# Optimization experiments

Measured on AMD Instinct MI355X. Metric: run time of the kernel, lower is better.

Reference implementation:

```python
import jax, jax.numpy as jnp
import numpy as np

DIM = 1536
HEADS = 12
HEAD_DIM = 128
SEQ = 3120
FRAME = 1560
EPS = 1e-6


def _rmsnorm(x, gamma, eps=EPS):
    var = jnp.mean(jnp.square(x), axis=-1, keepdims=True)
    return x * jax.lax.rsqrt(var + eps) * gamma


def _rope(x, cos, sin):
    # x: [B,S,H,D], cos/sin: [S, D//2]; rotate interleaved pairs (Wan-style)
    xr = x.reshape(x.shape[:-1] + (x.shape[-1] // 2, 2))
    x1, x2 = xr[..., 0], xr[..., 1]
    c = cos[None, :, None, :]
    s = sin[None, :, None, :]
    o1 = x1 * c - x2 * s
    o2 = x1 * s + x2 * c
    return jnp.stack([o1, o2], axis=-1).reshape(x.shape)


def setup_inputs() -> dict:
    key = jax.random.key(0)
    ks = jax.random.split(key, 8)
    pos = jnp.arange(SEQ, dtype=jnp.float32)[:, None]
    inv_freq = 1.0 / (10000.0 ** (jnp.arange(0, HEAD_DIM // 2, dtype=jnp.float32) / (HEAD_DIM // 2)))
    ang = pos * inv_freq[None, :]
    return {
        "hidden_states": jax.random.normal(ks[0], (1, SEQ, DIM), jnp.float32),
        "freqs_cos": jnp.cos(ang),
        "freqs_sin": jnp.sin(ang),
        "w_qkv": jax.random.normal(ks[1], (DIM, 3 * DIM), jnp.float32) * (DIM ** -0.5),
        "b_qkv": jnp.zeros((3 * DIM,), jnp.float32),
        "g_q": jnp.ones((DIM,), jnp.float32),
        "g_k": jnp.ones((DIM,), jnp.float32),
        "w_out": jax.random.normal(ks[2], (DIM, DIM), jnp.float32) * (DIM ** -0.5),
        "b_out": jnp.zeros((DIM,), jnp.float32),
        "frame_len": FRAME,
    }


def reference(hidden_states, freqs_cos, freqs_sin, w_qkv, b_qkv, g_q, g_k, w_out, b_out, frame_len):
    B, S, _ = hidden_states.shape
    qkv = hidden_states @ w_qkv + b_qkv  # [B,S,3*DIM]
    q, k, v = jnp.split(qkv, 3, axis=-1)
    q = _rmsnorm(q, g_q)
    k = _rmsnorm(k, g_k)
    q = q.reshape(B, S, HEADS, HEAD_DIM)
    k = k.reshape(B, S, HEADS, HEAD_DIM)
    v = v.reshape(B, S, HEADS, HEAD_DIM)
    q = _rope(q, freqs_cos, freqs_sin)
    k = _rope(k, freqs_cos, freqs_sin)
    # block-wise causal mask over frames of frame_len tokens
    blk = jnp.arange(S) // frame_len
    mask = blk[None, :] <= blk[:, None]  # [Sq, Sk]
    scale = 1.0 / jnp.sqrt(jnp.float32(HEAD_DIM))
    scores = jnp.einsum("bqhd,bkhd->bhqk", q, k) * scale
    scores = jnp.where(mask[None, None], scores, jnp.float32(-1e30))
    probs = jax.nn.softmax(scores, axis=-1)
    out = jnp.einsum("bhqk,bkhd->bqhd", probs, v)
    out = out.reshape(B, S, HEADS * HEAD_DIM)
    return out @ w_out + b_out
```

## Files before the change

### kernel.cpp

```cpp
#include <hip/hip_runtime.h>
#include <hip/hip_bf16.h>
#include <stdint.h>

#define SEQ_LEN 3120
#define DIM 1536
#define QKV_N 4608
#define HEADS 12
#define HEAD_DIM 128
#define FRAME_LEN 1560
#define SM_SCALE 0.08838834764831845f
#define LOG2E 1.4426950408889634f
#define FMAXC2 43.280851226669165f
#define BQ 256

#if __has_builtin(__builtin_amdgcn_exp2f)
#define FEXP2(x) __builtin_amdgcn_exp2f(x)
#else
#define FEXP2(x) exp2f(x)
#endif

typedef short short8 __attribute__((ext_vector_type(8)));
typedef float f32x4 __attribute__((ext_vector_type(4)));
typedef float f32x16 __attribute__((ext_vector_type(16)));

__device__ __forceinline__ unsigned short f2bf(float x) {
    union { float f; unsigned u; } v; v.f = x;
    unsigned r = v.u + 0x7fffu + ((v.u >> 16) & 1u);
    return (unsigned short)(r >> 16);
}
__device__ __forceinline__ float bf2f(unsigned short b) {
    union { unsigned u; float f; } v; v.u = ((unsigned)b) << 16;
    return v.f;
}
__device__ __forceinline__ unsigned pk2bf(float a, float b) {
    __hip_bfloat162 h = __float22bfloat162_rn(make_float2(a, b));
    union { __hip_bfloat162 h2; unsigned u; } v; v.h2 = h;
    return v.u;
}

__device__ __forceinline__ void async16(void* lds, const void* g) {
    __builtin_amdgcn_global_load_lds(
        (const __attribute__((address_space(1))) unsigned int*)g,
        (__attribute__((address_space(3))) unsigned int*)lds, 16, 0, 0);
}

__device__ __forceinline__ void transpose_tile(
    const float* __restrict__ in, unsigned short* __restrict__ out,
    int R, int C, int c0, int r0, float (*T)[65], int tid)
{
    const int rl = tid >> 4, cl = (tid & 15) * 4;
#pragma unroll
    for (int i = 0; i < 4; ++i) {
        const int row = r0 + rl + i * 16;
        float4 v = *(const float4*)&in[(size_t)row * C + c0 + cl];
        T[cl + 0][rl + i * 16] = v.x; T[cl + 1][rl + i * 16] = v.y;
        T[cl + 2][rl + i * 16] = v.z; T[cl + 3][rl + i * 16] = v.w;
    }
    __syncthreads();
    const int oc = tid >> 2, ob = (tid & 3) * 16;
    union { unsigned short t[16]; uint4 u[2]; } p;
#pragma unroll
    for (int j = 0; j < 16; ++j) p.t[j] = f2bf(T[oc][ob + j]);
    uint4* dst = (uint4*)&out[(size_t)(c0 + oc) * R + r0 + ob];
    dst[0] = p.u[0];
    dst[1] = p.u[1];
}

__global__ __launch_bounds__(256) void prep_kernel(
    const float* __restrict__ hs, unsigned short* __restrict__ hsb,
    const float* __restrict__ w_qkv, unsigned short* __restrict__ wqkvT,
    const float* __restrict__ w_out, unsigned short* __restrict__ woutT)
{
    __shared__ float T[64][65];
    const int bid = blockIdx.x;
    const int tid = threadIdx.x;
    if (bid < 2340) {
        const int i = bid * 256 + tid;
        const float4 a = ((const float4*)hs)[i * 2];
        const float4 b = ((const float4*)hs)[i * 2 + 1];
        union { unsigned short t[8]; uint4 u; } p;
        p.t[0] = f2bf(a.x); p.t[1] = f2bf(a.y); p.t[2] = f2bf(a.z); p.t[3] = f2bf(a.w);
        p.t[4] = f2bf(b.x); p.t[5] = f2bf(b.y); p.t[6] = f2bf(b.z); p.t[7] = f2bf(b.w);
        ((uint4*)hsb)[i] = p.u;
    } else if (bid < 4068) {
        const int t = bid - 2340;
        transpose_tile(w_qkv, wqkvT, DIM, QKV_N, (t % 72) * 64, (t / 72) * 64, T, tid);
    } else {
        const int t = bid - 4068;
        transpose_tile(w_out, woutT, DIM, DIM, (t % 24) * 64, (t / 24) * 64, T, tid);
    }
}

__global__ __launch_bounds__(256, 2) void gemm_bt_kernel(
    const unsigned short* __restrict__ A, const unsigned short* __restrict__ Bt,
    const float* __restrict__ bias, float* __restrict__ C, int M, int N, int K,
    int ntp, int spx)
{
    __shared__ short As[2][4096];
    __shared__ short Bs[2][4096];

    const int xcd = blockIdx.x & 7;
    const int idx = (xcd & 1) * spx + (blockIdx.x >> 3);
    const int mtiles = (M + 127) >> 7;
    if (idx >= ntp * mtiles) return;
    const int m0 = (idx / ntp) * 128;
    const int n0 = ((xcd >> 1) * ntp + idx % ntp) * 128;

    const int tid = threadIdx.x;
    const int w = tid >> 6, l = tid & 63;
    const int wr = w >> 1, wc = w & 1;
    const int lhi = l >> 4, llo = l & 15;

    f32x4 acc[4][4];
#pragma unroll
    for (int i = 0; i < 4; ++i)
#pragma unroll
        for (int j = 0; j < 4; ++j) acc[i][j] = f32x4{0.f, 0.f, 0.f, 0.f};

    const int c0i = (w * 2) * 64 + l, c1i = c0i + 64;
    const unsigned short* gA0 = A + (size_t)min(m0 + (c0i >> 2), M - 1) * K + (c0i & 3) * 8;
    const unsigned short* gA1 = A + (size_t)min(m0 + (c1i >> 2), M - 1) * K + (c1i & 3) * 8;
    const unsigned short* gB0 = Bt + (size_t)(n0 + (c0i >> 2)) * K + (c0i & 3) * 8;
    const unsigned short* gB1 = Bt + (size_t)(n0 + (c1i >> 2)) * K + (c1i & 3) * 8;

    const int aoff = (wr * 64 + llo) * 32 + lhi * 8;
    const int boff = (wc * 64 + llo) * 32 + lhi * 8;

    auto stage = [&](int k0, int b) {
        async16(As[b] + (w * 2 + 0) * 512, gA0 + k0);
        async16(As[b] + (w * 2 + 1) * 512, gA1 + k0);
        async16(Bs[b] + (w * 2 + 0) * 512, gB0 + k0);
        async16(Bs[b] + (w * 2 + 1) * 512, gB1 + k0);
    };

    const int nk = K >> 5;
    stage(0, 0);
    for (int t = 0; t < nk; ++t) {
        __syncthreads();
        if (t + 1 < nk) stage((t + 1) * 32, (t + 1) & 1);
        const short* A_ = As[t & 1];
        const short* B_ = Bs[t & 1];
        short8 af[4], bf[4];
#pragma unroll
        for (int mt = 0; mt < 4; ++mt) af[mt] = *(const short8*)&A_[aoff + mt * 512];
#pragma unroll
        for (int nt = 0; nt < 4; ++nt) bf[nt] = *(const short8*)&B_[boff + nt * 512];
#pragma unroll
        for (int mt = 0; mt < 4; ++mt)
#pragma unroll
            for (int nt = 0; nt < 4; ++nt)
                acc[mt][nt] = __builtin_amdgcn_mfma_f32_16x16x32_bf16(af[mt], bf[nt], acc[mt][nt], 0, 0, 0);
    }

#pragma unroll
    for (int mt = 0; mt < 4; ++mt)
#pragma unroll
        for (int ri = 0; ri < 4; ++ri) {
            const int row = m0 + wr * 64 + mt * 16 + lhi * 4 + ri;
            if (row < M) {
#pragma unroll
                for (int nt = 0; nt < 4; ++nt) {
                    const int col = n0 + wc * 64 + nt * 16 + llo;
                    C[(size_t)row * N + col] = acc[mt][nt][ri] + bias[col];
                }
            }
        }
}

__global__ __launch_bounds__(512, 2) void gemm256_bf16_kernel(
    const unsigned short* __restrict__ A, const unsigned short* __restrict__ Bt,
    const float* __restrict__ bias, unsigned short* __restrict__ C,
    int M, int N, int K)
{
    __shared__ short LDS[65536];

    const int mtiles = (M + 255) >> 8;
    const int nwg = mtiles * (N >> 8);
    const int q = nwg >> 3, r = nwg & 7;
    const int xcd = blockIdx.x & 7;
    const int g0 = (xcd < r) ? xcd * (q + 1) : r * (q + 1) + (xcd - r) * q;
    const int g = g0 + (int)(blockIdx.x >> 3);
    const int m0 = (g % mtiles) * 256;
    const int n0 = (g / mtiles) * 256;

    const int tid = threadIdx.x;
    const int w = tid >> 6, l = tid & 63;
    const int wr = w >> 2, wc = w & 3;
    const int lhi = l >> 4, llo = l & 15;

    f32x4 acc[8][4];
#pragma unroll
    for (int i = 0; i < 8; ++i)
#pragma unroll
        for (int j = 0; j < 4; ++j) acc[i][j] = f32x4{0.f, 0.f, 0.f, 0.f};

    const unsigned short* gsrc[8];
#pragma unroll
    for (int j = 0; j < 4; ++j) {
        const int c = (j * 8 + w) * 64 + l;
        const int row = c >> 3, ks = c & 7;
        gsrc[j] = A + (size_t)min(m0 + row, M - 1) * K + (ks ^ (row & 7)) * 8;
    }
#pragma unroll
    for (int j = 0; j < 4; ++j) {
        const int c = (j * 8 + w) * 64 + l;
        const int row = c >> 3, ks = c & 7;
        gsrc[4 + j] = Bt + (size_t)min(n0 + row, N - 1) * K + (ks ^ (row & 7)) * 8;
    }

    auto stageAll = [&](int kt, int b) {
        short* dst = LDS + b * 32768;
#pragma unroll
        for (int j = 0; j < 4; ++j)
            async16(dst + (j * 8 + w) * 512, gsrc[j] + kt * 64);
#pragma unroll
        for (int j = 0; j < 4; ++j)
            async16(dst + 16384 + (j * 8 + w) * 512, gsrc[4 + j] + kt * 64);
    };

    const int nk = K >> 6;
    stageAll(0, 0);
    asm volatile("s_waitcnt vmcnt(0)\n\ts_barrier" ::: "memory");

    for (int t = 0; t < nk; ++t) {
        if (t + 1 < nk) stageAll(t + 1, (t + 1) & 1);
        const short* Ab = LDS + (t & 1) * 32768;
        const short* Bb = Ab + 16384;
#pragma unroll
        for (int ph = 0; ph < 2; ++ph) {
            short8 bfr[4];
#pragma unroll
            for (int nt = 0; nt < 4; ++nt) {
                const int rb = wc * 64 + nt * 16 + llo;
                bfr[nt] = *(const short8*)&Bb[rb * 64 + ((ph * 4 + lhi) ^ (rb & 7)) * 8];
            }
#pragma unroll
            for (int mh = 0; mh < 2; ++mh) {
                short8 afr[4];
#pragma unroll
                for (int mt = 0; mt < 4; ++mt) {
                    const int ra = wr * 128 + mh * 64 + mt * 16 + llo;
                    afr[mt] = *(const short8*)&Ab[ra * 64 + ((ph * 4 + lhi) ^ (ra & 7)) * 8];
                }
                __builtin_amdgcn_s_setprio(1);
#pragma unroll
                for (int mt = 0; mt < 4; ++mt)
#pragma unroll
                    for (int nt = 0; nt < 4; ++nt)
                        acc[mh * 4 + mt][nt] = __builtin_amdgcn_mfma_f32_16x16x32_bf16(
                            afr[mt], bfr[nt], acc[mh * 4 + mt][nt], 0, 0, 0);
                __builtin_amdgcn_s_setprio(0);
            }
        }
        asm volatile("s_waitcnt vmcnt(0)\n\ts_barrier" ::: "memory");
    }

#pragma unroll
    for (int mi = 0; mi < 8; ++mi)
#pragma unroll
        for (int ri = 0; ri < 4; ++ri) {
            const int row = m0 + wr * 128 + mi * 16 + lhi * 4 + ri;
            if (row < M) {
#pragma unroll
                for (int nt = 0; nt < 4; ++nt) {
                    const int col = n0 + wc * 64 + nt * 16 + llo;
                    C[(size_t)row * N + col] = f2bf(acc[mi][nt][ri] + bias[col]);
                }
            }
        }
}

__global__ __launch_bounds__(256) void rmsrope_kernel(
    const unsigned short* __restrict__ qkvb, const float* __restrict__ gq,
    const float* __restrict__ gk, const float* __restrict__ cosf,
    const float* __restrict__ sinf, unsigned short* __restrict__ qb,
    unsigned short* __restrict__ kb)
{
    const int s = blockIdx.x;
    const int tid = threadIdx.x;
    const unsigned short* qrow = qkvb + (size_t)s * QKV_N;
    const unsigned short* krow = qrow + DIM;

    float2 qp[3], kp[3];
    float ssq_q = 0.f, ssq_k = 0.f;
#pragma unroll
    for (int j = 0; j < 3; ++j) {
        const int p = tid + j * 256;
        const unsigned uq = *(const unsigned*)(qrow + 2 * p);
        const unsigned uk = *(const unsigned*)(krow + 2 * p);
        qp[j] = make_float2(bf2f((unsigned short)(uq & 0xffff)), bf2f((unsigned short)(uq >> 16)));
        kp[j] = make_float2(bf2f((unsigned short)(uk & 0xffff)), bf2f((unsigned short)(uk >> 16)));
        ssq_q += qp[j].x * qp[j].x + qp[j].y * qp[j].y;
        ssq_k += kp[j].x * kp[j].x + kp[j].y * kp[j].y;
    }
#pragma unroll
    for (int off = 32; off > 0; off >>= 1) {
        ssq_q += __shfl_down(ssq_q, off);
        ssq_k += __shfl_down(ssq_k, off);
    }
    __shared__ float wq[4], wk[4];
    const int wave = tid >> 6, lane = tid & 63;
    if (lane == 0) { wq[wave] = ssq_q; wk[wave] = ssq_k; }
    __syncthreads();
    const float tq = wq[0] + wq[1] + wq[2] + wq[3];
    const float tk = wk[0] + wk[1] + wk[2] + wk[3];
    const float inv_q = rsqrtf(tq * (1.0f / DIM) + 1e-6f) * (SM_SCALE * LOG2E);
    const float inv_k = rsqrtf(tk * (1.0f / DIM) + 1e-6f);

#pragma unroll
    for (int j = 0; j < 3; ++j) {
        const int p = tid + j * 256;
        const int fi = p & 63;
        const float c = cosf[s * 64 + fi];
        const float si = sinf[s * 64 + fi];
        {
            const float y1 = qp[j].x * inv_q * gq[2 * p];
            const float y2 = qp[j].y * inv_q * gq[2 * p + 1];
            *(unsigned*)&qb[(size_t)s * DIM + 2 * p] = pk2bf(y1 * c - y2 * si, y1 * si + y2 * c);
        }
        {
            const float y1 = kp[j].x * inv_k * gk[2 * p];
            const float y2 = kp[j].y * inv_k * gk[2 * p + 1];
            *(unsigned*)&kb[(size_t)s * DIM + 2 * p] = pk2bf(y1 * c - y2 * si, y1 * si + y2 * c);
        }
    }
}

__global__ __launch_bounds__(256) void vtrans_kernel(
    const unsigned short* __restrict__ qkvb, unsigned short* __restrict__ vt)
{
    __shared__ float T[128][65];
    const int s0 = blockIdx.x * 64;
    const int h = blockIdx.y;
    const int tid = threadIdx.x;
    const int rl = tid >> 2, cb = (tid & 3) * 32;
    const int row = min(s0 + rl, SEQ_LEN - 1);
#pragma unroll
    for (int i = 0; i < 4; ++i) {
        const int d = cb + i * 8;
        union { uint4 u; unsigned short t[8]; } v;
        v.u = *(const uint4*)&qkvb[(size_t)row * QKV_N + 2 * DIM + h * HEAD_DIM + d];
#pragma unroll
        for (int j = 0; j < 8; ++j) T[d + j][rl] = bf2f(v.t[j]);
    }
    __syncthreads();
    const int od = tid >> 1, ob = (tid & 1) * 32;
    const size_t orow = (size_t)(h * HEAD_DIM + od) * SEQ_LEN;
#pragma unroll
    for (int v8 = 0; v8 < 4; ++v8) {
        const int s = s0 + ob + v8 * 8;
        if (s < SEQ_LEN) {
            union { unsigned short t[8]; uint4 u; } pk;
#pragma unroll
            for (int j = 0; j < 8; ++j) pk.t[j] = f2bf(T[od][ob + v8 * 8 + j]);
            *(uint4*)&vt[orow + s] = pk.u;
        }
    }
}

__global__ __launch_bounds__(512, 2) void attn_part_kernel(
    const unsigned short* __restrict__ qb, const unsigned short* __restrict__ kb,
    const unsigned short* __restrict__ vt, unsigned short* __restrict__ part_o,
    float* __restrict__ part_ml)
{
    __shared__ short KV[40960];

    const int bid = blockIdx.x;
    const int xcd = bid & 7;
    const int slot = bid >> 3;
    int h, bx;
    if (slot < 20) { h = xcd; bx = slot; }
    else { h = 8 + (xcd >> 1); bx = (xcd & 1) * 10 + (slot - 20); }

    const int tid = threadIdx.x;
    const int w = tid >> 6;
    const int l = tid & 63;
    int tile, split, nsp;
    if (bx < 6) { tile = bx; split = 0; nsp = 1; }
    else { const int b2 = bx - 6; tile = 6 + (b2 >> 1); split = b2 & 1; nsp = 2; }
    const int q0 = tile * BQ;
    const int lhi = l >> 5;
    const int llo = l & 31;

#pragma unroll
    for (int s = 0; s < 8; ++s) {
        const int c = (s * 8 + w) * 64 + l;
        const int row = c >> 4, g = c & 15;
        const int gr = min(q0 + row, SEQ_LEN - 1);
        async16(KV + (s * 8 + w) * 512, qb + (size_t)gr * DIM + h * HEAD_DIM + g * 8);
    }
    __syncthreads();
    short8 qf[8];
#pragma unroll
    for (int ds = 0; ds < 8; ++ds)
        qf[ds] = *(const short8*)&KV[(w * 32 + llo) * 128 + ds * 16 + lhi * 8];
    __syncthreads();

    const int myq = q0 + w * 32 + llo;
    const int mylimit = (myq < FRAME_LEN) ? FRAME_LEN : SEQ_LEN;
    const int wave_lim = (q0 + w * 32 < FRAME_LEN) ? FRAME_LEN : SEQ_LEN;
    const int Lmax = (tile < 6) ? FRAME_LEN : SEQ_LEN;
    const int nch = (Lmax + 63) >> 6;
    const int kc0 = ((split * nch) / nsp) * 64;
    const int kc1 = (((split + 1) * nch) / nsp) * 64;
    const int nchunks = (kc1 - kc0) >> 6;

    float l_run = 0.f;
    f32x16 o[4];
#pragma unroll
    for (int mt = 0; mt < 4; ++mt)
#pragma unroll
        for (int r = 0; r < 16; ++r) o[mt][r] = 0.f;

    int krloc[2], kcol[2], vcol[2], lof[2];
    size_t vrow[2];
#pragma unroll
    for (int s = 0; s < 2; ++s) {
        const int c = (s * 8 + w) * 64 + l;
        const int kr = c >> 4;
        krloc[s] = kr;
        kcol[s] = h * HEAD_DIM + (((c & 15) ^ (kr & 7)) * 8);
        const int d = c >> 3;
        vrow[s] = (size_t)(h * HEAD_DIM + d) * SEQ_LEN;
        vcol[s] = ((c & 7) ^ (d & 7)) * 8;
        lof[s] = (s * 8 + w) * 512;
    }

    auto issueK = [&](int kc, int b) {
#pragma unroll
        for (int s = 0; s < 2; ++s) {
            const int gr = min(kc + krloc[s], SEQ_LEN - 1);
            async16(KV + b * 8192 + lof[s], kb + (size_t)gr * DIM + kcol[s]);
        }
    };
    auto issueV = [&](int kc, int t) {
#pragma unroll
        for (int s = 0; s < 2; ++s) {
            const int col = min(kc + vcol[s], SEQ_LEN - 8);
            async16(KV + 16384 + t * 8192 + lof[s], vt + vrow[s] + col);
        }
    };

    auto qkt = [&](f32x16* st, int b) {
        const short* Kb = KV + b * 8192;
#pragma unroll
        for (int r = 0; r < 16; ++r) { st[0][r] = 0.f; st[1][r] = 0.f; }
#pragma unroll
        for (int ds = 0; ds < 8; ++ds) {
            const int gd = ds * 2 + lhi;
#pragma unroll
            for (int kt = 0; kt < 2; ++kt) {
                const int krow = kt * 32 + llo;
                short8 kf = *(const short8*)&Kb[krow * 128 + ((gd ^ (krow & 7)) * 8)];
                st[kt] = __builtin_amdgcn_mfma_f32_32x32x16_bf16(kf, qf[ds], st[kt], 0, 0, 0);
            }
        }
    };

    auto sm_pv = [&](f32x16* st, int kc, int t) {
        if (kc + 64 > wave_lim) {
#pragma unroll
            for (int kt = 0; kt < 2; ++kt)
#pragma unroll
                for (int r = 0; r < 16; ++r) {
                    const int kg = kc + kt * 32 + (r & 3) + 8 * (r >> 2) + 4 * lhi;
                    if (kg >= mylimit) st[kt][r] = -3.0e38f;
                }
        }
        float rs = 0.f;
        unsigned p16[2][8];
#pragma unroll
        for (int kt = 0; kt < 2; ++kt)
#pragma unroll
            for (int r2 = 0; r2 < 8; ++r2) {
                const float p0 = FEXP2(st[kt][2 * r2] - FMAXC2);
                const float p1 = FEXP2(st[kt][2 * r2 + 1] - FMAXC2);
                rs += p0 + p1;
                p16[kt][r2] = pk2bf(p0, p1);
            }
        l_run += rs;

        const short* Vb = KV + 16384 + t * 8192;
#pragma unroll
        for (int kblk = 0; kblk < 4; ++kblk) {
            const int tt = kblk >> 1;
            const int i0 = (kblk & 1) * 4;
            union { unsigned u[4]; short8 s8; } pf;
#if __has_builtin(__builtin_amdgcn_permlane32_swap)
            {
                auto s02 = __builtin_amdgcn_permlane32_swap(
                    p16[tt][i0 + 0], p16[tt][i0 + 2], false, false);
                auto s13 = __builtin_amdgcn_permlane32_swap(
                    p16[tt][i0 + 1], p16[tt][i0 + 3], false, false);
                pf.u[0] = s02[0]; pf.u[1] = s13[0];
                pf.u[2] = s02[1]; pf.u[3] = s13[1];
            }
#else
            {
                const int dk    = ((kblk & 1) * 2 + lhi) * 2;
                const int dsend = ((kblk & 1) * 2 + (1 - lhi)) * 2;
                const unsigned r0 = __shfl_xor(p16[tt][dsend], 32);
                const unsigned r1 = __shfl_xor(p16[tt][dsend + 1], 32);
                if (lhi == 0) { pf.u[0] = p16[tt][dk]; pf.u[1] = p16[tt][dk + 1]; pf.u[2] = r0; pf.u[3] = r1; }
                else          { pf.u[0] = r0; pf.u[1] = r1; pf.u[2] = p16[tt][dk]; pf.u[3] = p16[tt][dk + 1]; }
            }
#endif
#pragma unroll
            for (int mt = 0; mt < 4; ++mt) {
                const int vd = mt * 32 + llo;
                short8 vf = *(const short8*)&Vb[vd * 64 + (((kblk * 2 + lhi) ^ (vd & 7)) * 8)];
                o[mt] = __builtin_amdgcn_mfma_f32_32x32x16_bf16(vf, pf.s8, o[mt], 0, 0, 0);
            }
        }
    };

    issueK(kc0, 0); issueV(kc0, 0);
    if (nchunks > 1) { issueK(kc0 + 64, 1); issueV(kc0 + 64, 1); }
    __syncthreads();
    f32x16 stC[2];
    qkt(stC, 0);

    int vcur = 0;
    for (int i = 0, kc = kc0; i < nchunks; ++i, kc += 64) {
        __syncthreads();
        if (i + 2 < nchunks) {
            issueK(kc + 128, i & 1);
            int vt2 = vcur + 2; if (vt2 >= 3) vt2 -= 3;
            issueV(kc + 128, vt2);
        }
        f32x16 stN[2];
        if (i + 1 < nchunks) qkt(stN, (i + 1) & 1);
        sm_pv(stC, kc, vcur);
        if (i + 1 < nchunks) { stC[0] = stN[0]; stC[1] = stN[1]; }
        vcur = (vcur == 2) ? 0 : vcur + 1;
    }

    const float l_tot = l_run + __shfl_xor(l_run, 32);
    const int slot_o = bx * HEADS + h;
    const int qloc = w * 32 + llo;
    const float inv = (l_tot > 0.f) ? 1.0f / l_tot : 0.f;
    unsigned short* op = part_o + (size_t)slot_o * (BQ * HEAD_DIM) + qloc * HEAD_DIM + 4 * lhi;
#pragma unroll
    for (int mt = 0; mt < 4; ++mt)
#pragma unroll
        for (int g = 0; g < 4; ++g) {
            uint2 u;
            u.x = pk2bf(o[mt][4 * g + 0] * inv, o[mt][4 * g + 1] * inv);
            u.y = pk2bf(o[mt][4 * g + 2] * inv, o[mt][4 * g + 3] * inv);
            *(uint2*)&op[mt * 32 + 8 * g] = u;
        }
    if (lhi == 0) part_ml[(size_t)slot_o * BQ + qloc] = l_tot;
}

__global__ __launch_bounds__(256) void attn_combine_kernel(
    const unsigned short* __restrict__ part_o, const float* __restrict__ part_ml,
    unsigned short* __restrict__ attb)
{
    const int h = blockIdx.y;
    const int q = blockIdx.x * 8 + (threadIdx.x >> 5);
    const int dq = (threadIdx.x & 31) * 4;
    const int tile = q >> 8, qloc = q & 255;
    int base_bx, ns;
    if (tile < 6) { base_bx = tile; ns = 1; }
    else { base_bx = 6 + (tile - 6) * 2; ns = 2; }

    float W = 0.f;
    float acc[4] = {0.f, 0.f, 0.f, 0.f};
    for (int s = 0; s < ns; ++s) {
        const int slot = (base_bx + s) * HEADS + h;
        const float w = part_ml[(size_t)slot * BQ + qloc];
        if (w > 0.f) {
            W += w;
            const unsigned short* po = part_o +
                (size_t)slot * (BQ * HEAD_DIM) + qloc * HEAD_DIM + dq;
            uint2 u = *(const uint2*)po;
            acc[0] += w * bf2f((unsigned short)(u.x & 0xffff));
            acc[1] += w * bf2f((unsigned short)(u.x >> 16));
            acc[2] += w * bf2f((unsigned short)(u.y & 0xffff));
            acc[3] += w * bf2f((unsigned short)(u.y >> 16));
        }
    }
    const float inv = 1.0f / W;
    uint2 pk;
    pk.x = pk2bf(acc[0] * inv, acc[1] * inv);
    pk.y = pk2bf(acc[2] * inv, acc[3] * inv);
    *(uint2*)&attb[(size_t)q * DIM + h * HEAD_DIM + dq] = pk;
}

extern "C" void kernel_launch(void* const* d_in, const int* in_sizes, int n_in,
                              void* d_out, int out_size, void* d_ws, size_t ws_size,
                              hipStream_t stream)
{
    const float* hs    = (const float*)d_in[0];
    const float* cosf  = (const float*)d_in[1];
    const float* sinf  = (const float*)d_in[2];
    const float* w_qkv = (const float*)d_in[3];
    const float* b_qkv = (const float*)d_in[4];
    const float* g_q   = (const float*)d_in[5];
    const float* g_k   = (const float*)d_in[6];
    const float* w_out = (const float*)d_in[7];
    const float* b_out = (const float*)d_in[8];

    char* base = (char*)d_ws;
    unsigned short* qb     = (unsigned short*)base;
    unsigned short* kb     = (unsigned short*)(base + 9584640);
    unsigned short* vt     = (unsigned short*)(base + 19169280);
    unsigned short* hsb    = vt;
    unsigned short* qkvb   = (unsigned short*)(base + 28753920);
    unsigned short* part_o = (unsigned short*)(base + 28753920);
    float*          part_ml= (float*)(base + 60211200);
    unsigned short* wqkvT  = (unsigned short*)(base + 81469440);
    unsigned short* attb   = wqkvT;
    unsigned short* woutT  = (unsigned short*)(base + 95625216);
    float* outp = (float*)d_out;

    prep_kernel<<<4644, 256, 0, stream>>>(hs, hsb, w_qkv, wqkvT, w_out, woutT);
    gemm256_bf16_kernel<<<234, 512, 0, stream>>>(
        hsb, wqkvT, b_qkv, qkvb, SEQ_LEN, QKV_N, DIM);
    rmsrope_kernel<<<SEQ_LEN, 256, 0, stream>>>(qkvb, g_q, g_k, cosf, sinf, qb, kb);
    vtrans_kernel<<<dim3((SEQ_LEN + 63) / 64, HEADS), 256, 0, stream>>>(qkvb, vt);
    attn_part_kernel<<<240, 512, 0, stream>>>(qb, kb, vt, part_o, part_ml);
    attn_combine_kernel<<<dim3(SEQ_LEN / 8, HEADS), 256, 0, stream>>>(part_o, part_ml, attb);
    gemm_bt_kernel<<<304, 256, 0, stream>>>(
        attb, woutT, b_out, outp, SEQ_LEN, DIM, DIM, 3, 38);
}
```

Measured before the change: 284.6 us.

## Fuse rmsnorm-rope with V transpose, write unsplit attention tiles directly, add MFMA priority

Merges the RMSNorm+RoPE kernel and the V-transpose kernel into one launch. The transpose now keeps bf16 in shared memory instead of converting to float and back. Query tiles that are not split now write their normalized output straight into the attention buffer, so the combine kernel only runs over the split tiles. s_setprio is raised around the MFMA loops in the attention kernel. This removes one launch, roughly half the combine traffic, and partial-output round trips, at the cost of a more branchy fused kernel. Because attb aliases wqkvT, this also relies on the QKV weights no longer being needed by the time attention runs.

After: 280.1 us. Within noise of the previous version (-1.6%).

```diff
diff --git a/kernel.cpp b/kernel.cpp
--- a/kernel.cpp
+++ b/kernel.cpp
@@ -270,90 +270,90 @@
         }
 }
 
-__global__ __launch_bounds__(256) void rmsrope_kernel(
+__global__ __launch_bounds__(256) void rope_vt_kernel(
     const unsigned short* __restrict__ qkvb, const float* __restrict__ gq,
     const float* __restrict__ gk, const float* __restrict__ cosf,
     const float* __restrict__ sinf, unsigned short* __restrict__ qb,
-    unsigned short* __restrict__ kb)
-{
-    const int s = blockIdx.x;
+    unsigned short* __restrict__ kb, unsigned short* __restrict__ vt)
+{
+    __shared__ unsigned short T[128][72];
+    __shared__ float wq[4], wk[4];
+    const int bid = blockIdx.x;
     const int tid = threadIdx.x;
-    const unsigned short* qrow = qkvb + (size_t)s * QKV_N;
-    const unsigned short* krow = qrow + DIM;
-
-    float2 qp[3], kp[3];
-    float ssq_q = 0.f, ssq_k = 0.f;
-#pragma unroll
-    for (int j = 0; j < 3; ++j) {
-        const int p = tid + j * 256;
-        const unsigned uq = *(const unsigned*)(qrow + 2 * p);
-        const unsigned uk = *(const unsigned*)(krow + 2 * p);
-        qp[j] = make_float2(bf2f((unsigned short)(uq & 0xffff)), bf2f((unsigned short)(uq >> 16)));
-        kp[j] = make_float2(bf2f((unsigned short)(uk & 0xffff)), bf2f((unsigned short)(uk >> 16)));
-        ssq_q += qp[j].x * qp[j].x + qp[j].y * qp[j].y;
-        ssq_k += kp[j].x * kp[j].x + kp[j].y * kp[j].y;
-    }
-#pragma unroll
-    for (int off = 32; off > 0; off >>= 1) {
-        ssq_q += __shfl_down(ssq_q, off);
-        ssq_k += __shfl_down(ssq_k, off);
-    }
-    __shared__ float wq[4], wk[4];
-    const int wave = tid >> 6, lane = tid & 63;
-    if (lane == 0) { wq[wave] = ssq_q; wk[wave] = ssq_k; }
-    __syncthreads();
-    const float tq = wq[0] + wq[1] + wq[2] + wq[3];
-    const float tk = wk[0] + wk[1] + wk[2] + wk[3];
-    const float inv_q = rsqrtf(tq * (1.0f / DIM) + 1e-6f) * (SM_SCALE * LOG2E);
-    const float inv_k = rsqrtf(tk * (1.0f / DIM) + 1e-6f);
-
-#pragma unroll
-    for (int j = 0; j < 3; ++j) {
-        const int p = tid + j * 256;
-        const int fi = p & 63;
-        const float c = cosf[s * 64 + fi];
-        const float si = sinf[s * 64 + fi];
-        {
-            const float y1 = qp[j].x * inv_q * gq[2 * p];
-            const float y2 = qp[j].y * inv_q * gq[2 * p + 1];
-            *(unsigned*)&qb[(size_t)s * DIM + 2 * p] = pk2bf(y1 * c - y2 * si, y1 * si + y2 * c);
-        }
-        {
-            const float y1 = kp[j].x * inv_k * gk[2 * p];
-            const float y2 = kp[j].y * inv_k * gk[2 * p + 1];
-            *(unsigned*)&kb[(size_t)s * DIM + 2 * p] = pk2bf(y1 * c - y2 * si, y1 * si + y2 * c);
-        }
-    }
-}
-
-__global__ __launch_bounds__(256) void vtrans_kernel(
-    const unsigned short* __restrict__ qkvb, unsigned short* __restrict__ vt)
-{
-    __shared__ float T[128][65];
-    const int s0 = blockIdx.x * 64;
-    const int h = blockIdx.y;
-    const int tid = threadIdx.x;
-    const int rl = tid >> 2, cb = (tid & 3) * 32;
-    const int row = min(s0 + rl, SEQ_LEN - 1);
-#pragma unroll
-    for (int i = 0; i < 4; ++i) {
-        const int d = cb + i * 8;
-        union { uint4 u; unsigned short t[8]; } v;
-        v.u = *(const uint4*)&qkvb[(size_t)row * QKV_N + 2 * DIM + h * HEAD_DIM + d];
-#pragma unroll
-        for (int j = 0; j < 8; ++j) T[d + j][rl] = bf2f(v.t[j]);
-    }
-    __syncthreads();
-    const int od = tid >> 1, ob = (tid & 1) * 32;
-    const size_t orow = (size_t)(h * HEAD_DIM + od) * SEQ_LEN;
-#pragma unroll
-    for (int v8 = 0; v8 < 4; ++v8) {
-        const int s = s0 + ob + v8 * 8;
-        if (s < SEQ_LEN) {
-            union { unsigned short t[8]; uint4 u; } pk;
-#pragma unroll
-            for (int j = 0; j < 8; ++j) pk.t[j] = f2bf(T[od][ob + v8 * 8 + j]);
-            *(uint4*)&vt[orow + s] = pk.u;
+
+    if (bid < SEQ_LEN) {
+        const int s = bid;
+        const unsigned short* qrow = qkvb + (size_t)s * QKV_N;
+        const unsigned short* krow = qrow + DIM;
+
+        float2 qp[3], kp[3];
+        float ssq_q = 0.f, ssq_k = 0.f;
+#pragma unroll
+        for (int j = 0; j < 3; ++j) {
+            const int p = tid + j * 256;
+            const unsigned uq = *(const unsigned*)(qrow + 2 * p);
+            const unsigned uk = *(const unsigned*)(krow + 2 * p);
+            qp[j] = make_float2(bf2f((unsigned short)(uq & 0xffff)), bf2f((unsigned short)(uq >> 16)));
+            kp[j] = make_float2(bf2f((unsigned short)(uk & 0xffff)), bf2f((unsigned short)(uk >> 16)));
+            ssq_q += qp[j].x * qp[j].x + qp[j].y * qp[j].y;
+            ssq_k += kp[j].x * kp[j].x + kp[j].y * kp[j].y;
+        }
+#pragma unroll
+        for (int off = 32; off > 0; off >>= 1) {
+            ssq_q += __shfl_down(ssq_q, off);
+            ssq_k += __shfl_down(ssq_k, off);
+        }
+        const int wave = tid >> 6, lane = tid & 63;
+        if (lane == 0) { wq[wave] = ssq_q; wk[wave] = ssq_k; }
+        __syncthreads();
+        const float tq = wq[0] + wq[1] + wq[2] + wq[3];
+        const float tk = wk[0] + wk[1] + wk[2] + wk[3];
+        const float inv_q = rsqrtf(tq * (1.0f / DIM) + 1e-6f) * (SM_SCALE * LOG2E);
+        const float inv_k = rsqrtf(tk * (1.0f / DIM) + 1e-6f);
+
+#pragma unroll
+        for (int j = 0; j < 3; ++j) {
+            const int p = tid + j * 256;
+            const int fi = p & 63;
+            const float c = cosf[s * 64 + fi];
+            const float si = sinf[s * 64 + fi];
+            {
+                const float y1 = qp[j].x * inv_q * gq[2 * p];
+                const float y2 = qp[j].y * inv_q * gq[2 * p + 1];
+                *(unsigned*)&qb[(size_t)s * DIM + 2 * p] = pk2bf(y1 * c - y2 * si, y1 * si + y2 * c);
+            }
+            {
+                const float y1 = kp[j].x * inv_k * gk[2 * p];
+                const float y2 = kp[j].y * inv_k * gk[2 * p + 1];
+                *(unsigned*)&kb[(size_t)s * DIM + 2 * p] = pk2bf(y1 * c - y2 * si, y1 * si + y2 * c);
+            }
+        }
+    } else {
+        const int t = bid - SEQ_LEN;
+        const int s0 = (t % 49) * 64;
+        const int h = t / 49;
+        const int rl = tid >> 2, cb = (tid & 3) * 32;
+        const int row = min(s0 + rl, SEQ_LEN - 1);
+#pragma unroll
+        for (int i = 0; i < 4; ++i) {
+            const int d = cb + i * 8;
+            union { uint4 u; unsigned short t8[8]; } v;
+            v.u = *(const uint4*)&qkvb[(size_t)row * QKV_N + 2 * DIM + h * HEAD_DIM + d];
+#pragma unroll
+            for (int j = 0; j < 8; ++j) T[d + j][rl] = v.t8[j];
+        }
+        __syncthreads();
+        const int od = tid >> 1, ob = (tid & 1) * 32;
+        const size_t orow = (size_t)(h * HEAD_DIM + od) * SEQ_LEN;
+#pragma unroll
+        for (int v8 = 0; v8 < 4; ++v8) {
+            const int s = s0 + ob + v8 * 8;
+            if (s < SEQ_LEN) {
+                union { unsigned short t8[8]; uint4 u; } pk;
+#pragma unroll
+                for (int j = 0; j < 8; ++j) pk.t8[j] = T[od][ob + v8 * 8 + j];
+                *(uint4*)&vt[orow + s] = pk.u;
+            }
         }
     }
 }
@@ -361,7 +361,7 @@
 __global__ __launch_bounds__(512, 2) void attn_part_kernel(
     const unsigned short* __restrict__ qb, const unsigned short* __restrict__ kb,
     const unsigned short* __restrict__ vt, unsigned short* __restrict__ part_o,
-    float* __restrict__ part_ml)
+    float* __restrict__ part_ml, unsigned short* __restrict__ attb)
 {
     __shared__ short KV[40960];
 
@@ -445,6 +445,7 @@
         const short* Kb = KV + b * 8192;
 #pragma unroll
         for (int r = 0; r < 16; ++r) { st[0][r] = 0.f; st[1][r] = 0.f; }
+        __builtin_amdgcn_s_setprio(1);
 #pragma unroll
         for (int ds = 0; ds < 8; ++ds) {
             const int gd = ds * 2 + lhi;
@@ -455,6 +456,7 @@
                 st[kt] = __builtin_amdgcn_mfma_f32_32x32x16_bf16(kf, qf[ds], st[kt], 0, 0, 0);
             }
         }
+        __builtin_amdgcn_s_setprio(0);
     };
 
     auto sm_pv = [&](f32x16* st, int kc, int t) {
@@ -505,12 +507,14 @@
                 else          { pf.u[0] = r0; pf.u[1] = r1; pf.u[2] = p16[tt][dk]; pf.u[3] = p16[tt][dk + 1]; }
             }
 #endif
+            __builtin_amdgcn_s_setprio(1);
 #pragma unroll
             for (int mt = 0; mt < 4; ++mt) {
                 const int vd = mt * 32 + llo;
                 short8 vf = *(const short8*)&Vb[vd * 64 + (((kblk * 2 + lhi) ^ (vd & 7)) * 8)];
                 o[mt] = __builtin_amdgcn_mfma_f32_32x32x16_bf16(vf, pf.s8, o[mt], 0, 0, 0);
             }
+            __builtin_amdgcn_s_setprio(0);
         }
     };
 
@@ -536,20 +540,33 @@
     }
 
     const float l_tot = l_run + __shfl_xor(l_run, 32);
-    const int slot_o = bx * HEADS + h;
     const int qloc = w * 32 + llo;
     const float inv = (l_tot > 0.f) ? 1.0f / l_tot : 0.f;
-    unsigned short* op = part_o + (size_t)slot_o * (BQ * HEAD_DIM) + qloc * HEAD_DIM + 4 * lhi;
-#pragma unroll
-    for (int mt = 0; mt < 4; ++mt)
-#pragma unroll
-        for (int g = 0; g < 4; ++g) {
-            uint2 u;
-            u.x = pk2bf(o[mt][4 * g + 0] * inv, o[mt][4 * g + 1] * inv);
-            u.y = pk2bf(o[mt][4 * g + 2] * inv, o[mt][4 * g + 3] * inv);
-            *(uint2*)&op[mt * 32 + 8 * g] = u;
-        }
-    if (lhi == 0) part_ml[(size_t)slot_o * BQ + qloc] = l_tot;
+    if (nsp == 1) {
+        unsigned short* op = attb + (size_t)(q0 + qloc) * DIM + h * HEAD_DIM + 4 * lhi;
+#pragma unroll
+        for (int mt = 0; mt < 4; ++mt)
+#pragma unroll
+            for (int g = 0; g < 4; ++g) {
+                uint2 u;
+                u.x = pk2bf(o[mt][4 * g + 0] * inv, o[mt][4 * g + 1] * inv);
+                u.y = pk2bf(o[mt][4 * g + 2] * inv, o[mt][4 * g + 3] * inv);
+                *(uint2*)&op[mt * 32 + 8 * g] = u;
+            }
+    } else {
+        const int slot_o = bx * HEADS + h;
+        unsigned short* op = part_o + (size_t)slot_o * (BQ * HEAD_DIM) + qloc * HEAD_DIM + 4 * lhi;
+#pragma unroll
+        for (int mt = 0; mt < 4; ++mt)
+#pragma unroll
+            for (int g = 0; g < 4; ++g) {
+                uint2 u;
+                u.x = pk2bf(o[mt][4 * g + 0] * inv, o[mt][4 * g + 1] * inv);
+                u.y = pk2bf(o[mt][4 * g + 2] * inv, o[mt][4 * g + 3] * inv);
+                *(uint2*)&op[mt * 32 + 8 * g] = u;
+            }
+        if (lhi == 0) part_ml[(size_t)slot_o * BQ + qloc] = l_tot;
+    }
 }
 
 __global__ __launch_bounds__(256) void attn_combine_kernel(
@@ -557,16 +574,15 @@
     unsigned short* __restrict__ attb)
 {
     const int h = blockIdx.y;
-    const int q = blockIdx.x * 8 + (threadIdx.x >> 5);
+    const int q = 1536 + blockIdx.x * 8 + (threadIdx.x >> 5);
     const int dq = (threadIdx.x & 31) * 4;
     const int tile = q >> 8, qloc = q & 255;
-    int base_bx, ns;
-    if (tile < 6) { base_bx = tile; ns = 1; }
-    else { base_bx = 6 + (tile - 6) * 2; ns = 2; }
+    const int base_bx = 6 + (tile - 6) * 2;
 
     float W = 0.f;
     float acc[4] = {0.f, 0.f, 0.f, 0.f};
-    for (int s = 0; s < ns; ++s) {
+#pragma unroll
+    for (int s = 0; s < 2; ++s) {
         const int slot = (base_bx + s) * HEADS + h;
         const float w = part_ml[(size_t)slot * BQ + qloc];
         if (w > 0.f) {
@@ -617,10 +633,11 @@
     prep_kernel<<<4644, 256, 0, stream>>>(hs, hsb, w_qkv, wqkvT, w_out, woutT);
     gemm256_bf16_kernel<<<234, 512, 0, stream>>>(
         hsb, wqkvT, b_qkv, qkvb, SEQ_LEN, QKV_N, DIM);
-    rmsrope_kernel<<<SEQ_LEN, 256, 0, stream>>>(qkvb, g_q, g_k, cosf, sinf, qb, kb);
-    vtrans_kernel<<<dim3((SEQ_LEN + 63) / 64, HEADS), 256, 0, stream>>>(qkvb, vt);
-    attn_part_kernel<<<240, 512, 0, stream>>>(qb, kb, vt, part_o, part_ml);
-    attn_combine_kernel<<<dim3(SEQ_LEN / 8, HEADS), 256, 0, stream>>>(part_o, part_ml, attb);
+    rope_vt_kernel<<<SEQ_LEN + 49 * HEADS, 256, 0, stream>>>(
+        qkvb, g_q, g_k, cosf, sinf, qb, kb, vt);
+    attn_part_kernel<<<240, 512, 0, stream>>>(qb, kb, vt, part_o, part_ml, attb);
+    attn_combine_kernel<<<dim3((SEQ_LEN - 1536) / 8, HEADS), 256, 0, stream>>>(
+        part_o, part_ml, attb);
     gemm_bt_kernel<<<304, 256, 0, stream>>>(
         attb, woutT, b_out, outp, SEQ_LEN, DIM, DIM, 3, 38);
 }
```
